# Performance work log

Hardware: AMD Instinct MI355X
Metric: run time of the kernel (lower is better)

Reference implementation:

```python
import jax, jax.numpy as jnp
import numpy as np

D = 2048
H = 16
DK = D // H
B = 2
S = 2048


def setup_inputs() -> dict:
    key = jax.random.key(0)
    ks = jax.random.split(key, 11)
    s = 1.0 / np.sqrt(D)
    inp = {
        "q": jax.random.normal(ks[0], (B, S, D), jnp.float32),
        "k": jax.random.normal(ks[1], (B, S, D), jnp.float32),
        "v": jax.random.normal(ks[2], (B, S, D), jnp.float32),
        "mask": 0,
        "Wq": jax.random.normal(ks[3], (D, D), jnp.float32) * s,
        "bq": jax.random.normal(ks[4], (D,), jnp.float32) * s,
        "Wk": jax.random.normal(ks[5], (D, D), jnp.float32) * s,
        "bk": jax.random.normal(ks[6], (D,), jnp.float32) * s,
        "Wv": jax.random.normal(ks[7], (D, D), jnp.float32) * s,
        "bv": jax.random.normal(ks[8], (D,), jnp.float32) * s,
        "Wo": jax.random.normal(ks[9], (D, D), jnp.float32) * s,
        "bo": jax.random.normal(ks[10], (D,), jnp.float32) * s,
    }
    return inp


def reference(q, k, v, mask, Wq, bq, Wk, bk, Wv, bv, Wo, bo):
    # Linear projections (torch Linear: x @ W.T + b)
    query = q @ Wq.T + bq  # [B,S,D]
    key_ = k @ Wk.T + bk
    value = v @ Wv.T + bv
    # split heads -> [B,S,H,DK]
    query = query.reshape(B, S, H, DK)
    key_ = key_.reshape(B, S, H, DK)
    value = value.reshape(B, S, H, DK)
    # scores [B,H,Sq,Sk]
    scores = jnp.einsum('nqhd,nkhd->nhqk', query, key_)
    if mask:
        # faithful to source: fill where triu(ones, diag=1) == 0 (lower tri incl diag)
        tri = jnp.triu(jnp.ones((S, S), jnp.float32), k=1)
        scores = jnp.where(tri == 0, jnp.float32(-1e20), scores)
    attn = jax.nn.softmax(scores / np.sqrt(DK), axis=3)
    # dropout=0.0 -> identity
    out = jnp.einsum('nhql,nlhd->nqhd', attn, value).reshape(B, S, D)
    return out @ Wo.T + bo
```

## Files before the change

kernel.cpp:

```cpp
#include <hip/hip_runtime.h>
#include <math.h>

typedef unsigned short u16;
typedef u16 u16x8 __attribute__((ext_vector_type(8)));
typedef u16 u16x4 __attribute__((ext_vector_type(4)));
typedef short s16x8 __attribute__((ext_vector_type(8)));
typedef short s16x4 __attribute__((ext_vector_type(4)));
typedef float f32x4 __attribute__((ext_vector_type(4)));

static constexpr int B_ = 2;
static constexpr int S_ = 2048;
static constexpr int D_ = 2048;
static constexpr int H_ = 16;
static constexpr int DK = 128;
static constexpr long long BSD = (long long)B_ * S_ * D_;
static constexpr long long DD  = (long long)D_ * D_;

#if __has_builtin(__builtin_amdgcn_mfma_f32_16x16x32_bf16)
#define HAVE_MFMA32 1
#else
#define HAVE_MFMA32 0
#endif
#if __has_builtin(__builtin_amdgcn_mfma_f32_16x16x16bf16_1k)
#define HAVE_MFMA16 1
#else
#define HAVE_MFMA16 0
#endif

__device__ __forceinline__ u16 f2bf(float f) {
    union { float f; unsigned u; } cv; cv.f = f;
    unsigned u = cv.u;
    return (u16)((u + 0x7fffu + ((u >> 16) & 1u)) >> 16);
}

__device__ __forceinline__ unsigned pack2bf(float a, float b) {
    union { float f; unsigned u; } x, y; x.f = a; y.f = b;
    return ((y.u + 0x8000u) & 0xffff0000u) | ((x.u + 0x8000u) >> 16);
}

__device__ __forceinline__ f32x4 mfma32(f32x4 c, u16x8 a, u16x8 b) {
#if HAVE_MFMA32
    return __builtin_amdgcn_mfma_f32_16x16x32_bf16((s16x8)a, (s16x8)b, c, 0, 0, 0);
#else
    asm volatile("v_mfma_f32_16x16x32_bf16 %0, %1, %2, %0" : "+v"(c) : "v"(a), "v"(b));
    return c;
#endif
}
__device__ __forceinline__ f32x4 mfma16(f32x4 c, u16x4 a, u16x4 b) {
#if HAVE_MFMA16
    return __builtin_amdgcn_mfma_f32_16x16x16bf16_1k((s16x4)a, (s16x4)b, c, 0, 0, 0);
#else
    asm volatile("v_mfma_f32_16x16x16_bf16 %0, %1, %2, %0" : "+v"(c) : "v"(a), "v"(b));
    return c;
#endif
}
__device__ __forceinline__ void fenceB() {
#if !HAVE_MFMA32 || !HAVE_MFMA16
    asm volatile("s_nop 7\ns_nop 7" :::);
#endif
}

__device__ __forceinline__ void glds16(const u16* g, u16* l) {
    __builtin_amdgcn_global_load_lds(
        (const __attribute__((address_space(1))) unsigned int*)g,
        (__attribute__((address_space(3))) unsigned int*)l, 16, 0, 0);
}

__device__ __forceinline__ float fexp2(float x) {
#if __has_builtin(__builtin_amdgcn_exp2f)
    return __builtin_amdgcn_exp2f(x);
#else
    return exp2f(x);
#endif
}

__device__ __forceinline__ void cfence() { asm volatile("" ::: "memory"); }
__device__ __forceinline__ void barrier8() {
    cfence();
    __builtin_amdgcn_s_barrier();
    cfence();
}
#define LGKM0() do { asm volatile("s_waitcnt lgkmcnt(0)" ::: "memory"); \
                     __builtin_amdgcn_sched_barrier(0); } while (0)
#define VMC(N)  asm volatile("s_waitcnt vmcnt(" #N ")" ::: "memory")

struct CastArgs {
    const float* src[7];
    u16* dst[7];
    int start[8];
};
__global__ __launch_bounds__(256) void cast_all(CastArgs a) {
    int g = blockIdx.x * 256 + threadIdx.x;
    if (g >= a.start[7]) return;
    int seg = 0;
#pragma unroll
    for (int i = 1; i < 7; ++i) seg += (g >= a.start[i]) ? 1 : 0;
    int idx = g - a.start[seg];
    float4 f = ((const float4*)a.src[seg])[idx];
    ushort4 o;
    o.x = f2bf(f.x); o.y = f2bf(f.y); o.z = f2bf(f.z); o.w = f2bf(f.w);
    ((ushort4*)a.dst[seg])[idx] = o;
}

#define GEMM_K64_LOOP(Aptr, Bptr)                                                   \
    for (int k0 = 0; k0 < D_; k0 += 64) {                                           \
        __syncthreads();                                                            \
        _Pragma("unroll")                                                           \
        for (int s = 0; s < 4; ++s) {                                               \
            int slot = s * 256 + t;                                                 \
            int row = slot >> 3;                                                    \
            int c = (t & 7) ^ (row & 7);                                            \
            glds16(Aptr + (m0 + row) * D_ + k0 + c * 8, &As[slot * 8]);             \
        }                                                                           \
        _Pragma("unroll")                                                           \
        for (int s = 0; s < 4; ++s) {                                               \
            int slot = s * 256 + t;                                                 \
            int row = slot >> 3;                                                    \
            int c = (t & 7) ^ (row & 7);                                            \
            glds16(Bptr + (n0 + row) * D_ + k0 + c * 8, &Bs[slot * 8]);             \
        }                                                                           \
        __syncthreads();                                                            \
        u16x8 af[4][2], bf[4][2];                                                   \
        _Pragma("unroll")                                                           \
        for (int i = 0; i < 4; ++i) {                                               \
            int row = wm + i * 16 + l16;                                            \
            _Pragma("unroll")                                                       \
            for (int kk = 0; kk < 2; ++kk)                                          \
                af[i][kk] = *(const u16x8*)(&As[row * 64 +                          \
                                (((kk * 4 + quad) ^ (row & 7)) * 8)]);              \
        }                                                                           \
        _Pragma("unroll")                                                           \
        for (int j = 0; j < 4; ++j) {                                               \
            int row = wn + j * 16 + l16;                                            \
            _Pragma("unroll")                                                       \
            for (int kk = 0; kk < 2; ++kk)                                          \
                bf[j][kk] = *(const u16x8*)(&Bs[row * 64 +                          \
                                (((kk * 4 + quad) ^ (row & 7)) * 8)]);              \
        }                                                                           \
        _Pragma("unroll")                                                           \
        for (int kk = 0; kk < 2; ++kk)                                              \
            _Pragma("unroll")                                                       \
            for (int i = 0; i < 4; ++i)                                             \
                _Pragma("unroll")                                                   \
                for (int j = 0; j < 4; ++j)                                         \
                    acc[i][j] = mfma32(acc[i][j], af[i][kk], bf[j][kk]);            \
    }

struct QkvArgs {
    const u16* X[3];
    const u16* W[3];
    const float* bias[3];
    u16* outQ;
    u16* outK;
    u16* outVt;
    float scaleQ;
};

#define STAGE_U(LDSP, GBASE)                                                        \
    _Pragma("unroll")                                                               \
    for (int jj = 0; jj < 2; ++jj) {                                                \
        int slot = jj * 512 + t;                                                    \
        int row = slot >> 3, c = slot & 7;                                          \
        glds16((GBASE) + (long long)row * D_ + ((c ^ (row & 7)) * 8),               \
               (LDSP) + slot * 8);                                                  \
    }

#define RD_K(kk, AsT, BsT)                                                          \
    _Pragma("unroll")                                                               \
    for (int i2 = 0; i2 < 4; ++i2) {                                                \
        int row = wm64 + i2 * 16 + l16;                                             \
        af2[i2] = *(const u16x8*)(&(AsT)[row * 64 +                                 \
                        ((((kk) * 4 + quad) ^ (row & 7)) * 8)]);                    \
    }                                                                               \
    _Pragma("unroll")                                                               \
    for (int j2 = 0; j2 < 4; ++j2) {                                                \
        int row = wn64 + j2 * 16 + l16;                                             \
        bf2[j2] = *(const u16x8*)(&(BsT)[row * 64 +                                 \
                        ((((kk) * 4 + quad) ^ (row & 7)) * 8)]);                    \
    }

#define MMK()                                                                       \
    __builtin_amdgcn_s_setprio(1);                                                  \
    _Pragma("unroll")                                                               \
    for (int i2 = 0; i2 < 4; ++i2)                                                  \
        _Pragma("unroll")                                                           \
        for (int j2 = 0; j2 < 4; ++j2)                                              \
            acc[i2][j2] = mfma32(acc[i2][j2], af2[i2], bf2[j2]);                    \
    __builtin_amdgcn_s_setprio(0);

__global__ __launch_bounds__(512, 2) void qkv_tri(QkvArgs a) {
    __shared__ u16 SM8[73728];
    u16* const Abase = SM8;
    u16* const Bbase = SM8 + 24576;

    const int l = blockIdx.x;
    const int f = (l & 7) * 96 + (l >> 3);
    const int zsel = f >> 8;
    const int r = f & 255;
    const int bx = r >> 5;
    const int by = r & 31;

    const u16* __restrict__ Ag = a.X[zsel];
    const u16* __restrict__ Bg = a.W[zsel];

    const int t = threadIdx.x;
    const int lane = t & 63;
    const int quad = lane >> 4, l16 = lane & 15;
    const int wave = t >> 6;
    const int wm64 = (wave >> 2) * 64;
    const int wn64 = (wave & 3) * 64;
    const long long m0 = (long long)by * 128;
    const long long n0 = (long long)bx * 256;

    f32x4 acc[4][4];
#pragma unroll
    for (int i = 0; i < 4; ++i)
#pragma unroll
        for (int j = 0; j < 4; ++j)
            acc[i][j] = f32x4{0.f, 0.f, 0.f, 0.f};

    u16x8 af2[4], bf2[4];

    STAGE_U(Abase,                Ag + m0 * D_)
    STAGE_U(Bbase,                Bg + n0 * D_)
    STAGE_U(Bbase + 8192,         Bg + (n0 + 128) * D_)
    STAGE_U(Abase + 8192,         Ag + m0 * D_ + 64)
    STAGE_U(Bbase + 16384,        Bg + n0 * D_ + 64)
    STAGE_U(Bbase + 16384 + 8192, Bg + (n0 + 128) * D_ + 64)
    VMC(6);
    barrier8();

    int eb = 0, ob = 1;
#pragma unroll 1
    for (int it = 0; it < 16; ++it) {
        const bool more = (it < 15);
        const long long kE2 = (long long)(2 * it + 2) * 64;
        const long long kO2 = kE2 + 64;
        const int en = (eb + 2 > 2) ? eb - 1 : eb + 2;

        u16* const AsE = Abase + eb * 8192;
        u16* const BsE = Bbase + eb * 16384;
        u16* const AsO = Abase + ob * 8192;
        u16* const BsO = Bbase + ob * 16384;
        u16* const AsnE = Abase + en * 8192;
        u16* const BsnE = Bbase + en * 16384;
        u16* const AsnO = AsE;
        u16* const BsnO = BsE;

        RD_K(0, AsE, BsE)
        if (more) {
            STAGE_U(AsnE, Ag + m0 * D_ + kE2)
            STAGE_U(BsnE, Bg + n0 * D_ + kE2)
        }
        barrier8(); LGKM0(); MMK() barrier8();

        RD_K(1, AsE, BsE)
        if (more) { STAGE_U(BsnE + 8192, Bg + (n0 + 128) * D_ + kE2) }
        barrier8(); LGKM0(); MMK()
        if (more) { VMC(6); } else { VMC(0); }
        barrier8();

        RD_K(0, AsO, BsO)
        if (more) {
            STAGE_U(AsnO, Ag + m0 * D_ + kO2)
            STAGE_U(BsnO, Bg + n0 * D_ + kO2)
        }
        barrier8(); LGKM0(); MMK() barrier8();

        RD_K(1, AsO, BsO)
        if (more) { STAGE_U(BsnO + 8192, Bg + (n0 + 128) * D_ + kO2) }
        barrier8(); LGKM0(); MMK()
        if (more) { VMC(6); }
        barrier8();

        eb = en;
        ob = (ob + 2 > 2) ? ob - 1 : ob + 2;
    }
    fenceB();

    float bs[4];
#pragma unroll
    for (int j = 0; j < 4; ++j)
        bs[j] = a.bias[zsel][(int)n0 + wn64 + j * 16 + l16];

    if (zsel < 2) {
        const float scale = (zsel == 0) ? a.scaleQ : 1.0f;
        u16* C = (zsel == 0) ? a.outQ : a.outK;
#pragma unroll
        for (int i = 0; i < 4; ++i)
#pragma unroll
            for (int j = 0; j < 4; ++j)
#pragma unroll
                for (int rr = 0; rr < 4; ++rr) {
                    int row = wm64 + i * 16 + quad * 4 + rr;
                    int col = wn64 + j * 16 + l16;
                    SM8[row * 256 + col] = f2bf((acc[i][j][rr] + bs[j]) * scale);
                }
        barrier8();
#pragma unroll
        for (int s = 0; s < 8; ++s) {
            int idx = s * 512 + t;
            int row = idx >> 5, c = idx & 31;
            *(u16x8*)(C + (m0 + row) * (long long)D_ + n0 + c * 8) =
                *(const u16x8*)(&SM8[row * 256 + c * 8]);
        }
    } else {
        const int h0 = (int)(n0 >> 7);
        const int bb = (int)(m0 >> 11);
        const int tok0 = (int)(m0 & 2047);
#pragma unroll
        for (int i = 0; i < 4; ++i)
#pragma unroll
            for (int j = 0; j < 4; ++j)
#pragma unroll
                for (int rr = 0; rr < 4; ++rr) {
                    int row = wm64 + i * 16 + quad * 4 + rr;
                    int d = wn64 + j * 16 + l16;
                    SM8[d * 136 + row] = f2bf(acc[i][j][rr] + bs[j]);
                }
        barrier8();
#pragma unroll
        for (int hh = 0; hh < 2; ++hh) {
            u16* vt = a.outVt + (long long)(bb * 16 + h0 + hh) * DK * S_;
#pragma unroll
            for (int s = 0; s < 4; ++s) {
                int idx = s * 512 + t;
                int d = idx >> 4, tc = idx & 15;
                *(u16x8*)(vt + (long long)d * S_ + tok0 + tc * 8) =
                    *(const u16x8*)(&SM8[(hh * 128 + d) * 136 + tc * 8]);
            }
        }
    }
}

__global__ __launch_bounds__(256) void gemm_out(const u16* __restrict__ Ain,
                                                const u16* __restrict__ Bin,
                                                float* __restrict__ C,
                                                const float* __restrict__ bias) {
    __shared__ u16 SM[16384];
    u16* As = SM;
    u16* Bs = SM + 8192;

    const int t = threadIdx.x;
    const int wave = t >> 6, lane = t & 63;
    const int quad = lane >> 4, l16 = lane & 15;
    const int wm = (wave >> 1) * 64;
    const int wn = (wave & 1) * 64;
    const long long m0 = (long long)blockIdx.y * 128;
    const long long n0 = (long long)blockIdx.x * 128;

    f32x4 acc[4][4];
#pragma unroll
    for (int i = 0; i < 4; ++i)
#pragma unroll
        for (int j = 0; j < 4; ++j)
            acc[i][j] = f32x4{0.f, 0.f, 0.f, 0.f};

    GEMM_K64_LOOP(Ain, Bin)

    fenceB();

    float bs[4];
#pragma unroll
    for (int j = 0; j < 4; ++j)
        bs[j] = bias[(int)n0 + wn + j * 16 + l16];

    float* Cf = (float*)SM;
#pragma unroll
    for (int p = 0; p < 2; ++p) {
        __syncthreads();
#pragma unroll
        for (int jj = 0; jj < 2; ++jj) {
            int j = p * 2 + jj;
#pragma unroll
            for (int i = 0; i < 4; ++i)
#pragma unroll
                for (int r = 0; r < 4; ++r) {
                    int row = wm + i * 16 + quad * 4 + r;
                    int lc = (wave & 1) * 32 + jj * 16 + l16;
                    Cf[row * 64 + lc] = acc[i][j][r] + bs[j];
                }
        }
        __syncthreads();
#pragma unroll
        for (int i = 0; i < 8; ++i) {
            int idx = i * 256 + t;
            int row = idx >> 4, c4 = idx & 15;
            f32x4 val = *(const f32x4*)(&Cf[row * 64 + c4 * 4]);
            long long n = n0 + (c4 >> 3) * 64 + p * 32 + (c4 & 7) * 4;
            *(f32x4*)(C + (m0 + row) * (long long)D_ + n) = val;
        }
    }
}

__global__ __launch_bounds__(256, 2) void flash_attn(const u16* __restrict__ Qb,
                                                     const u16* __restrict__ Kb,
                                                     const u16* __restrict__ Vt,
                                                     u16* __restrict__ Ob) {
    __shared__ u16 Ks[2][64 * 128];
    __shared__ u16 Vs[2][128 * 64];

    const int z  = blockIdx.x;
    const int qt = blockIdx.y;
    const int b  = z >> 4, h = z & 15;
    const int t = threadIdx.x, wave = t >> 6, lane = t & 63;
    const int quad = lane >> 4, l16 = lane & 15;

    const u16* kbase = Kb + (long long)(b * S_) * D_ + h * DK;
    const u16* vbase = Vt + (long long)z * DK * S_;

    u16x8 qf[2][4];
    {
        const u16* qbase = Qb + ((long long)(b * S_ + qt * 128 + wave * 32 + l16)) * D_
                              + h * DK + quad * 8;
#pragma unroll
        for (int jq = 0; jq < 2; ++jq)
#pragma unroll
            for (int kk = 0; kk < 4; ++kk)
                qf[jq][kk] = *(const u16x8*)(qbase + (long long)jq * 16 * D_ + kk * 32);
    }

    f32x4 acc_o[2][8];
#pragma unroll
    for (int jq = 0; jq < 2; ++jq)
#pragma unroll
        for (int jd = 0; jd < 8; ++jd)
            acc_o[jq][jd] = f32x4{0.f, 0.f, 0.f, 0.f};
    float l_[2] = {0.f, 0.f};

    u16x8 vreg[4];

    {
#pragma unroll
        for (int i = 0; i < 4; ++i) {
            int slot = i * 256 + t;
            int row = slot >> 3, c16 = slot & 7;
            vreg[i] = *(const u16x8*)(vbase + (long long)row * S_ + c16 * 8);
        }
#pragma unroll
        for (int i = 0; i < 4; ++i) {
            int slot = i * 256 + t;
            int row = slot >> 4;
            int cs = (slot & 15) ^ (row & 7);
            glds16(kbase + (long long)row * D_ + cs * 8, &Ks[0][slot * 8]);
        }
#pragma unroll
        for (int i = 0; i < 4; ++i) {
            int slot = i * 256 + t;
            int row = slot >> 3, c16 = slot & 7;
            int rm = row & 15;
            u16x4 lo = __builtin_shufflevector(vreg[i], vreg[i], 0, 1, 2, 3);
            u16x4 hi = __builtin_shufflevector(vreg[i], vreg[i], 4, 5, 6, 7);
            *(u16x4*)(&Vs[0][row * 64 + (((2 * c16) ^ rm) * 4)]) = lo;
            *(u16x4*)(&Vs[0][row * 64 + (((2 * c16 + 1) ^ rm) * 4)]) = hi;
        }
    }

    for (int kt = 0; kt < S_ / 64; ++kt) {
        __syncthreads();
        const int p = kt & 1;
        const u16* ks = Ks[p];
        const u16* vs = Vs[p];
        const bool pre = (kt + 1) < (S_ / 64);
        if (pre) {
            const u16* vsrc = vbase + (kt + 1) * 64;
#pragma unroll
            for (int i = 0; i < 4; ++i) {
                int slot = i * 256 + t;
                int row = slot >> 3, c16 = slot & 7;
                vreg[i] = *(const u16x8*)(vsrc + (long long)row * S_ + c16 * 8);
            }
            const u16* ksrc = kbase + (long long)(kt + 1) * 64 * D_;
#pragma unroll
            for (int i = 0; i < 4; ++i) {
                int slot = i * 256 + t;
                int row = slot >> 4;
                int cs = (slot & 15) ^ (row & 7);
                glds16(ksrc + (long long)row * D_ + cs * 8, &Ks[p ^ 1][slot * 8]);
            }
        }

        f32x4 st[4][2];
#pragma unroll
        for (int ik = 0; ik < 4; ++ik)
#pragma unroll
            for (int jq = 0; jq < 2; ++jq)
                st[ik][jq] = f32x4{0.f, 0.f, 0.f, 0.f};
#pragma unroll
        for (int kk = 0; kk < 4; ++kk) {
            u16x8 kf[4];
#pragma unroll
            for (int ik = 0; ik < 4; ++ik) {
                int krow = ik * 16 + l16;
                kf[ik] = *(const u16x8*)(&ks[krow * 128 + (((kk * 4 + quad) ^ (l16 & 7)) * 8)]);
            }
#pragma unroll
            for (int ik = 0; ik < 4; ++ik) {
                st[ik][0] = mfma32(st[ik][0], kf[ik], qf[0][kk]);
                st[ik][1] = mfma32(st[ik][1], kf[ik], qf[1][kk]);
            }
        }
        fenceB();

        if (pre) {
#pragma unroll
            for (int i = 0; i < 4; ++i) {
                int slot = i * 256 + t;
                int row = slot >> 3, c16 = slot & 7;
                int rm = row & 15;
                u16x4 lo = __builtin_shufflevector(vreg[i], vreg[i], 0, 1, 2, 3);
                u16x4 hi = __builtin_shufflevector(vreg[i], vreg[i], 4, 5, 6, 7);
                *(u16x4*)(&Vs[p ^ 1][row * 64 + (((2 * c16) ^ rm) * 4)]) = lo;
                *(u16x4*)(&Vs[p ^ 1][row * 64 + (((2 * c16 + 1) ^ rm) * 4)]) = hi;
            }
        }

        u16x4 pf[4][2];
#pragma unroll
        for (int ik = 0; ik < 4; ++ik)
#pragma unroll
            for (int jq = 0; jq < 2; ++jq) {
                float p0 = fexp2(st[ik][jq][0]);
                float p1 = fexp2(st[ik][jq][1]);
                float p2 = fexp2(st[ik][jq][2]);
                float p3 = fexp2(st[ik][jq][3]);
                l_[jq] += (p0 + p1) + (p2 + p3);
                union { u16x4 v; unsigned u[2]; } pk;
                pk.u[0] = pack2bf(p0, p1);
                pk.u[1] = pack2bf(p2, p3);
                pf[ik][jq] = pk.v;
            }

#pragma unroll
        for (int ik = 0; ik < 4; ++ik) {
            const int kc = ik * 4 + quad;
            u16x4 vf[8];
#pragma unroll
            for (int jd = 0; jd < 8; ++jd) {
                int vrow = jd * 16 + l16;
                vf[jd] = *(const u16x4*)(&vs[vrow * 64 + ((kc ^ l16) * 4)]);
            }
#pragma unroll
            for (int jd = 0; jd < 8; ++jd) {
                acc_o[0][jd] = mfma16(acc_o[0][jd], pf[ik][0], vf[jd]);
                acc_o[1][jd] = mfma16(acc_o[1][jd], pf[ik][1], vf[jd]);
            }
        }
        fenceB();
    }

    float lr[2][4];
#pragma unroll
    for (int jq = 0; jq < 2; ++jq) {
        float s = l_[jq];
        s += __shfl_xor(s, 16, 64);
        s += __shfl_xor(s, 32, 64);
        float inv = 1.f / s;
#pragma unroll
        for (int r = 0; r < 4; ++r)
            lr[jq][r] = __shfl(inv, quad * 20 + r, 64);
    }
    u16* OS = (u16*)Ks;
    __syncthreads();
#pragma unroll
    for (int jq = 0; jq < 2; ++jq)
#pragma unroll
        for (int r = 0; r < 4; ++r) {
            int qloc = wave * 32 + jq * 16 + quad * 4 + r;
#pragma unroll
            for (int jd = 0; jd < 8; ++jd)
                OS[qloc * 128 + jd * 16 + l16] = f2bf(acc_o[jq][jd][r] * lr[jq][r]);
        }
    __syncthreads();
    u16* obase = Ob + ((long long)(b * S_ + qt * 128)) * D_ + h * DK;
#pragma unroll
    for (int i = 0; i < 8; ++i) {
        int idx = i * 256 + t;
        int row = idx >> 4, cc = idx & 15;
        *(u16x8*)(obase + (long long)row * D_ + cc * 8) = *(const u16x8*)(&OS[row * 128 + cc * 8]);
    }
}

extern "C" void kernel_launch(void* const* d_in, const int* in_sizes, int n_in,
                              void* d_out, int out_size, void* d_ws, size_t ws_size,
                              hipStream_t stream) {
    const float* q  = (const float*)d_in[0];
    const float* k  = (const float*)d_in[1];
    const float* v  = (const float*)d_in[2];
    const float* Wq = (const float*)d_in[4];
    const float* bq = (const float*)d_in[5];
    const float* Wk = (const float*)d_in[6];
    const float* bk = (const float*)d_in[7];
    const float* Wv = (const float*)d_in[8];
    const float* bv = (const float*)d_in[9];
    const float* Wo = (const float*)d_in[10];
    const float* bo = (const float*)d_in[11];
    float* out = (float*)d_out;

    u16* ws = (u16*)d_ws;
    u16* xq  = ws; ws += BSD;
    u16* xk  = ws; ws += BSD;
    u16* xv  = ws; ws += BSD;
    u16* wqb = ws; ws += DD;
    u16* wkb = ws; ws += DD;
    u16* wvb = ws; ws += DD;
    u16* wob = ws; ws += DD;
    u16* Qb  = ws; ws += BSD;
    u16* Kb  = ws; ws += BSD;
    u16* Vt  = ws; ws += BSD;
    u16* Ob  = ws; ws += BSD;

    const float q_scale = (float)(0.08838834764831845 * 1.4426950408889634);

    {
        CastArgs a;
        const float* srcs[7] = {q, k, v, Wq, Wk, Wv, Wo};
        u16* dsts[7] = {xq, xk, xv, wqb, wkb, wvb, wob};
        int n4s[7] = {(int)(BSD / 4), (int)(BSD / 4), (int)(BSD / 4),
                      (int)(DD / 4), (int)(DD / 4), (int)(DD / 4), (int)(DD / 4)};
        int acc = 0;
        for (int i = 0; i < 7; ++i) { a.src[i] = srcs[i]; a.dst[i] = dsts[i]; a.start[i] = acc; acc += n4s[i]; }
        a.start[7] = acc;
        cast_all<<<(acc + 255) / 256, 256, 0, stream>>>(a);
    }

    {
        QkvArgs a;
        a.X[0] = xq;  a.X[1] = xk;  a.X[2] = xv;
        a.W[0] = wqb; a.W[1] = wkb; a.W[2] = wvb;
        a.bias[0] = bq; a.bias[1] = bk; a.bias[2] = bv;
        a.outQ = Qb; a.outK = Kb; a.outVt = Vt;
        a.scaleQ = q_scale;
        qkv_tri<<<dim3(768, 1, 1), 512, 0, stream>>>(a);
    }

    flash_attn<<<dim3(B_ * H_, S_ / 128), 256, 0, stream>>>(Qb, Kb, Vt, Ob);

    gemm_out<<<dim3(D_ / 128, (B_ * S_) / 128), 256, 0, stream>>>(Ob, wob, out, bo);
}
```

Baseline: 434.3 us.

## Share a leaner triple-buffered GEMM mainloop between QKV and output projections

Replaces the QKV GEMM's unrolled two-phase loop, which had many barriers, with a shared macro body. The body uses one barrier per K-step, precomputed swizzled LDS offsets, incremented global pointers, and a three-stage async-copy pipeline. The output projection moves from a simple single-buffered 128x128 GEMM with 256 threads to the same 128x256, 512-thread pipelined body with a grouped block-index remap for L2 locality. It trades larger LDS use and lower occupancy for fewer synchronizations and better load/compute overlap.

```diff
diff --git a/kernel.cpp b/kernel.cpp
--- a/kernel.cpp
+++ b/kernel.cpp
@@ -80,9 +80,8 @@
     __builtin_amdgcn_s_barrier();
     cfence();
 }
-#define LGKM0() do { asm volatile("s_waitcnt lgkmcnt(0)" ::: "memory"); \
-                     __builtin_amdgcn_sched_barrier(0); } while (0)
 #define VMC(N)  asm volatile("s_waitcnt vmcnt(" #N ")" ::: "memory")
+#define LGKMB() do { asm volatile("s_waitcnt lgkmcnt(0)" ::: "memory"); barrier8(); } while (0)
 
 struct CastArgs {
     const float* src[7];
@@ -102,49 +101,107 @@
     ((ushort4*)a.dst[seg])[idx] = o;
 }
 
-#define GEMM_K64_LOOP(Aptr, Bptr)                                                   \
-    for (int k0 = 0; k0 < D_; k0 += 64) {                                           \
-        __syncthreads();                                                            \
+
+#define ABYTE(s) ((s) * 16384)
+#define BBYTE(s) (49152 + (s) * 32768)
+
+#define STAGE_TILE(SA, SB)                                                          \
+    glds16(pA0, SMu + ((SA) >> 1) + d0);                                            \
+    glds16(pA1, SMu + ((SA) >> 1) + d1);                                            \
+    glds16(pB00, SMu + ((SB) >> 1) + d0);                                           \
+    glds16(pB01, SMu + ((SB) >> 1) + d1);                                           \
+    glds16(pB10, SMu + ((SB) >> 1) + 8192 + d0);                                    \
+    glds16(pB11, SMu + ((SB) >> 1) + 8192 + d1);                                    \
+    pA0 += 64; pA1 += 64; pB00 += 64; pB01 += 64; pB10 += 64; pB11 += 64;
+
+#define LD8(BOFF) (*(const u16x8*)(SMc + (BOFF)))
+
+#define RD_FRAGS(SA, SB)                                                            \
+    _Pragma("unroll")                                                               \
+    for (int i2 = 0; i2 < 4; ++i2) {                                                \
+        afA[i2] = LD8((SA) + offA[i2]);                                             \
+        afB[i2] = LD8((SA) + (offA[i2] ^ 64));                                      \
+    }                                                                               \
+    _Pragma("unroll")                                                               \
+    for (int j2 = 0; j2 < 4; ++j2) {                                                \
+        bfA[j2] = LD8((SB) + offB[j2]);                                             \
+        bfB[j2] = LD8((SB) + (offB[j2] ^ 64));                                      \
+    }
+
+#define MMALL()                                                                     \
+    __builtin_amdgcn_s_setprio(1);                                                  \
+    _Pragma("unroll")                                                               \
+    for (int i2 = 0; i2 < 4; ++i2)                                                  \
         _Pragma("unroll")                                                           \
-        for (int s = 0; s < 4; ++s) {                                               \
-            int slot = s * 256 + t;                                                 \
-            int row = slot >> 3;                                                    \
-            int c = (t & 7) ^ (row & 7);                                            \
-            glds16(Aptr + (m0 + row) * D_ + k0 + c * 8, &As[slot * 8]);             \
-        }                                                                           \
+        for (int j2 = 0; j2 < 4; ++j2)                                              \
+            acc[i2][j2] = mfma32(acc[i2][j2], afA[i2], bfA[j2]);                    \
+    _Pragma("unroll")                                                               \
+    for (int i2 = 0; i2 < 4; ++i2)                                                  \
         _Pragma("unroll")                                                           \
-        for (int s = 0; s < 4; ++s) {                                               \
-            int slot = s * 256 + t;                                                 \
-            int row = slot >> 3;                                                    \
-            int c = (t & 7) ^ (row & 7);                                            \
-            glds16(Bptr + (n0 + row) * D_ + k0 + c * 8, &Bs[slot * 8]);             \
-        }                                                                           \
-        __syncthreads();                                                            \
-        u16x8 af[4][2], bf[4][2];                                                   \
+        for (int j2 = 0; j2 < 4; ++j2)                                              \
+            acc[i2][j2] = mfma32(acc[i2][j2], afB[i2], bfB[j2]);                    \
+    __builtin_amdgcn_s_setprio(0);
+
+#define GEMM_LEAN_BODY(AGPTR, BGPTR)                                                \
+    u16* const SMu = SM8;                                                           \
+    const char* const SMc = (const char*)SM8;                                       \
+    const int t = threadIdx.x;                                                      \
+    const int lane = t & 63;                                                        \
+    const int quad = lane >> 4, l16 = lane & 15;                                    \
+    const int wave = t >> 6;                                                        \
+    const int wm64 = (wave >> 2) * 64;                                              \
+    const int wn64 = (wave & 3) * 64;                                               \
+    const long long m0 = (long long)by * 128;                                       \
+    const long long n0 = (long long)bx * 256;                                       \
+    const int tr = t >> 3, tc = t & 7;                                              \
+    const int swz = (tc ^ (tr & 7)) * 8;                                            \
+    const u16* pA0  = (AGPTR) + (m0 + tr) * D_ + swz;                               \
+    const u16* pA1  = (AGPTR) + (m0 + 64 + tr) * D_ + swz;                          \
+    const u16* pB00 = (BGPTR) + (n0 + tr) * D_ + swz;                               \
+    const u16* pB01 = (BGPTR) + (n0 + 64 + tr) * D_ + swz;                          \
+    const u16* pB10 = (BGPTR) + (n0 + 128 + tr) * D_ + swz;                         \
+    const u16* pB11 = (BGPTR) + (n0 + 192 + tr) * D_ + swz;                         \
+    const int d0 = t * 8, d1 = t * 8 + 4096;                                        \
+    int offA[4], offB[4];                                                           \
+    _Pragma("unroll")                                                               \
+    for (int i2 = 0; i2 < 4; ++i2) {                                                \
+        int rowA = wm64 + i2 * 16 + l16;                                            \
+        offA[i2] = rowA * 128 + ((quad ^ (rowA & 7)) << 4);                         \
+        int rowB = wn64 + i2 * 16 + l16;                                            \
+        offB[i2] = rowB * 128 + ((quad ^ (rowB & 7)) << 4);                         \
+    }                                                                               \
+    f32x4 acc[4][4];                                                                \
+    _Pragma("unroll")                                                               \
+    for (int i = 0; i < 4; ++i)                                                     \
         _Pragma("unroll")                                                           \
-        for (int i = 0; i < 4; ++i) {                                               \
-            int row = wm + i * 16 + l16;                                            \
-            _Pragma("unroll")                                                       \
-            for (int kk = 0; kk < 2; ++kk)                                          \
-                af[i][kk] = *(const u16x8*)(&As[row * 64 +                          \
-                                (((kk * 4 + quad) ^ (row & 7)) * 8)]);              \
-        }                                                                           \
-        _Pragma("unroll")                                                           \
-        for (int j = 0; j < 4; ++j) {                                               \
-            int row = wn + j * 16 + l16;                                            \
-            _Pragma("unroll")                                                       \
-            for (int kk = 0; kk < 2; ++kk)                                          \
-                bf[j][kk] = *(const u16x8*)(&Bs[row * 64 +                          \
-                                (((kk * 4 + quad) ^ (row & 7)) * 8)]);              \
-        }                                                                           \
-        _Pragma("unroll")                                                           \
-        for (int kk = 0; kk < 2; ++kk)                                              \
-            _Pragma("unroll")                                                       \
-            for (int i = 0; i < 4; ++i)                                             \
-                _Pragma("unroll")                                                   \
-                for (int j = 0; j < 4; ++j)                                         \
-                    acc[i][j] = mfma32(acc[i][j], af[i][kk], bf[j][kk]);            \
-    }
+        for (int j = 0; j < 4; ++j)                                                 \
+            acc[i][j] = f32x4{0.f, 0.f, 0.f, 0.f};                                  \
+    u16x8 afA[4], afB[4], bfA[4], bfB[4];                                           \
+                                            \
+    STAGE_TILE(ABYTE(0), BBYTE(0))                                                  \
+    STAGE_TILE(ABYTE(1), BBYTE(1))                                                  \
+    VMC(6);                                                                         \
+    barrier8();                                                                     \
+    _Pragma("unroll 3")                                                             \
+    for (int kt = 0; kt < 30; ++kt) {                                               \
+        const int s = kt % 3;                                                       \
+        const int s2 = (kt + 2) % 3;                                                \
+        RD_FRAGS(ABYTE(s), BBYTE(s))                                                \
+        STAGE_TILE(ABYTE(s2), BBYTE(s2))                                            \
+        MMALL()                                                                     \
+        VMC(6);                                                                     \
+        LGKMB();                                                                    \
+    }                                                                               \
+                             \
+    RD_FRAGS(ABYTE(0), BBYTE(0))                                                    \
+    MMALL()                                                                         \
+    VMC(0);                                                                         \
+    LGKMB();                                                                        \
+                                                              \
+    RD_FRAGS(ABYTE(1), BBYTE(1))                                                    \
+    MMALL()                                                                         \
+    LGKMB();                                                                        \
+    fenceB();
 
 struct QkvArgs {
     const u16* X[3];
@@ -156,127 +213,20 @@
     float scaleQ;
 };
 
-#define STAGE_U(LDSP, GBASE)                                                        \
-    _Pragma("unroll")                                                               \
-    for (int jj = 0; jj < 2; ++jj) {                                                \
-        int slot = jj * 512 + t;                                                    \
-        int row = slot >> 3, c = slot & 7;                                          \
-        glds16((GBASE) + (long long)row * D_ + ((c ^ (row & 7)) * 8),               \
-               (LDSP) + slot * 8);                                                  \
-    }
-
-#define RD_K(kk, AsT, BsT)                                                          \
-    _Pragma("unroll")                                                               \
-    for (int i2 = 0; i2 < 4; ++i2) {                                                \
-        int row = wm64 + i2 * 16 + l16;                                             \
-        af2[i2] = *(const u16x8*)(&(AsT)[row * 64 +                                 \
-                        ((((kk) * 4 + quad) ^ (row & 7)) * 8)]);                    \
-    }                                                                               \
-    _Pragma("unroll")                                                               \
-    for (int j2 = 0; j2 < 4; ++j2) {                                                \
-        int row = wn64 + j2 * 16 + l16;                                             \
-        bf2[j2] = *(const u16x8*)(&(BsT)[row * 64 +                                 \
-                        ((((kk) * 4 + quad) ^ (row & 7)) * 8)]);                    \
-    }
-
-#define MMK()                                                                       \
-    __builtin_amdgcn_s_setprio(1);                                                  \
-    _Pragma("unroll")                                                               \
-    for (int i2 = 0; i2 < 4; ++i2)                                                  \
-        _Pragma("unroll")                                                           \
-        for (int j2 = 0; j2 < 4; ++j2)                                              \
-            acc[i2][j2] = mfma32(acc[i2][j2], af2[i2], bf2[j2]);                    \
-    __builtin_amdgcn_s_setprio(0);
-
-__global__ __launch_bounds__(512, 2) void qkv_tri(QkvArgs a) {
+__global__ __launch_bounds__(512, 2) void qkv_lean(QkvArgs a) {
     __shared__ u16 SM8[73728];
-    u16* const Abase = SM8;
-    u16* const Bbase = SM8 + 24576;
 
     const int l = blockIdx.x;
-    const int f = (l & 7) * 96 + (l >> 3);
-    const int zsel = f >> 8;
-    const int r = f & 255;
-    const int bx = r >> 5;
-    const int by = r & 31;
+    const int zsel = l >> 8;
+    const int pi = l & 7;
+    const int cc_ = (l >> 3) & 31;
+    const int by = (pi & 3) * 8 + (cc_ & 7);
+    const int bx = ((pi >> 2) << 2) + (cc_ >> 3);
 
     const u16* __restrict__ Ag = a.X[zsel];
     const u16* __restrict__ Bg = a.W[zsel];
 
-    const int t = threadIdx.x;
-    const int lane = t & 63;
-    const int quad = lane >> 4, l16 = lane & 15;
-    const int wave = t >> 6;
-    const int wm64 = (wave >> 2) * 64;
-    const int wn64 = (wave & 3) * 64;
-    const long long m0 = (long long)by * 128;
-    const long long n0 = (long long)bx * 256;
-
-    f32x4 acc[4][4];
-#pragma unroll
-    for (int i = 0; i < 4; ++i)
-#pragma unroll
-        for (int j = 0; j < 4; ++j)
-            acc[i][j] = f32x4{0.f, 0.f, 0.f, 0.f};
-
-    u16x8 af2[4], bf2[4];
-
-    STAGE_U(Abase,                Ag + m0 * D_)
-    STAGE_U(Bbase,                Bg + n0 * D_)
-    STAGE_U(Bbase + 8192,         Bg + (n0 + 128) * D_)
-    STAGE_U(Abase + 8192,         Ag + m0 * D_ + 64)
-    STAGE_U(Bbase + 16384,        Bg + n0 * D_ + 64)
-    STAGE_U(Bbase + 16384 + 8192, Bg + (n0 + 128) * D_ + 64)
-    VMC(6);
-    barrier8();
-
-    int eb = 0, ob = 1;
-#pragma unroll 1
-    for (int it = 0; it < 16; ++it) {
-        const bool more = (it < 15);
-        const long long kE2 = (long long)(2 * it + 2) * 64;
-        const long long kO2 = kE2 + 64;
-        const int en = (eb + 2 > 2) ? eb - 1 : eb + 2;
-
-        u16* const AsE = Abase + eb * 8192;
-        u16* const BsE = Bbase + eb * 16384;
-        u16* const AsO = Abase + ob * 8192;
-        u16* const BsO = Bbase + ob * 16384;
-        u16* const AsnE = Abase + en * 8192;
-        u16* const BsnE = Bbase + en * 16384;
-        u16* const AsnO = AsE;
-        u16* const BsnO = BsE;
-
-        RD_K(0, AsE, BsE)
-        if (more) {
-            STAGE_U(AsnE, Ag + m0 * D_ + kE2)
-            STAGE_U(BsnE, Bg + n0 * D_ + kE2)
-        }
-        barrier8(); LGKM0(); MMK() barrier8();
-
-        RD_K(1, AsE, BsE)
-        if (more) { STAGE_U(BsnE + 8192, Bg + (n0 + 128) * D_ + kE2) }
-        barrier8(); LGKM0(); MMK()
-        if (more) { VMC(6); } else { VMC(0); }
-        barrier8();
-
-        RD_K(0, AsO, BsO)
-        if (more) {
-            STAGE_U(AsnO, Ag + m0 * D_ + kO2)
-            STAGE_U(BsnO, Bg + n0 * D_ + kO2)
-        }
-        barrier8(); LGKM0(); MMK() barrier8();
-
-        RD_K(1, AsO, BsO)
-        if (more) { STAGE_U(BsnO + 8192, Bg + (n0 + 128) * D_ + kO2) }
-        barrier8(); LGKM0(); MMK()
-        if (more) { VMC(6); }
-        barrier8();
-
-        eb = en;
-        ob = (ob + 2 > 2) ? ob - 1 : ob + 2;
-    }
-    fenceB();
+    GEMM_LEAN_BODY(Ag, Bg)
 
     float bs[4];
 #pragma unroll
@@ -325,70 +275,57 @@
 #pragma unroll
             for (int s = 0; s < 4; ++s) {
                 int idx = s * 512 + t;
-                int d = idx >> 4, tc = idx & 15;
-                *(u16x8*)(vt + (long long)d * S_ + tok0 + tc * 8) =
-                    *(const u16x8*)(&SM8[(hh * 128 + d) * 136 + tc * 8]);
-            }
-        }
-    }
-}
-
-__global__ __launch_bounds__(256) void gemm_out(const u16* __restrict__ Ain,
-                                                const u16* __restrict__ Bin,
-                                                float* __restrict__ C,
-                                                const float* __restrict__ bias) {
-    __shared__ u16 SM[16384];
-    u16* As = SM;
-    u16* Bs = SM + 8192;
-
-    const int t = threadIdx.x;
-    const int wave = t >> 6, lane = t & 63;
-    const int quad = lane >> 4, l16 = lane & 15;
-    const int wm = (wave >> 1) * 64;
-    const int wn = (wave & 1) * 64;
-    const long long m0 = (long long)blockIdx.y * 128;
-    const long long n0 = (long long)blockIdx.x * 128;
-
-    f32x4 acc[4][4];
-#pragma unroll
-    for (int i = 0; i < 4; ++i)
-#pragma unroll
-        for (int j = 0; j < 4; ++j)
-            acc[i][j] = f32x4{0.f, 0.f, 0.f, 0.f};
-
-    GEMM_K64_LOOP(Ain, Bin)
-
-    fenceB();
+                int d = idx >> 4, tcc = idx & 15;
+                *(u16x8*)(vt + (long long)d * S_ + tok0 + tcc * 8) =
+                    *(const u16x8*)(&SM8[(hh * 128 + d) * 136 + tcc * 8]);
+            }
+        }
+    }
+}
+
+__global__ __launch_bounds__(512, 2) void gemm_out_lean(const u16* __restrict__ Ain,
+                                                        const u16* __restrict__ Bin,
+                                                        float* __restrict__ C,
+                                                        const float* __restrict__ bias) {
+    __shared__ u16 SM8[73728];
+
+    const int l = blockIdx.x;
+    const int pi = l & 7;
+    const int cc_ = (l >> 3) & 31;
+    const int by = (pi & 3) * 8 + (cc_ & 7);
+    const int bx = ((pi >> 2) << 2) + (cc_ >> 3);
+
+    GEMM_LEAN_BODY(Ain, Bin)
 
     float bs[4];
 #pragma unroll
     for (int j = 0; j < 4; ++j)
-        bs[j] = bias[(int)n0 + wn + j * 16 + l16];
-
-    float* Cf = (float*)SM;
+        bs[j] = bias[(int)n0 + wn64 + j * 16 + l16];
+
+    float* Cf = (float*)SM8;
 #pragma unroll
     for (int p = 0; p < 2; ++p) {
-        __syncthreads();
-#pragma unroll
-        for (int jj = 0; jj < 2; ++jj) {
-            int j = p * 2 + jj;
+        barrier8();
+        if (((wave & 3) >> 1) == p) {
+            int wnl = (wave & 1) * 64;
 #pragma unroll
             for (int i = 0; i < 4; ++i)
 #pragma unroll
-                for (int r = 0; r < 4; ++r) {
-                    int row = wm + i * 16 + quad * 4 + r;
-                    int lc = (wave & 1) * 32 + jj * 16 + l16;
-                    Cf[row * 64 + lc] = acc[i][j][r] + bs[j];
-                }
-        }
-        __syncthreads();
-#pragma unroll
-        for (int i = 0; i < 8; ++i) {
-            int idx = i * 256 + t;
-            int row = idx >> 4, c4 = idx & 15;
-            f32x4 val = *(const f32x4*)(&Cf[row * 64 + c4 * 4]);
-            long long n = n0 + (c4 >> 3) * 64 + p * 32 + (c4 & 7) * 4;
-            *(f32x4*)(C + (m0 + row) * (long long)D_ + n) = val;
+                for (int j = 0; j < 4; ++j)
+#pragma unroll
+                    for (int rr = 0; rr < 4; ++rr) {
+                        int row = wm64 + i * 16 + quad * 4 + rr;
+                        int lc = wnl + j * 16 + l16;
+                        Cf[row * 128 + lc] = acc[i][j][rr] + bs[j];
+                    }
+        }
+        barrier8();
+#pragma unroll
+        for (int s = 0; s < 8; ++s) {
+            int idx = s * 512 + t;
+            int row = idx >> 5, c4 = idx & 31;
+            f32x4 val = *(const f32x4*)(&Cf[row * 128 + c4 * 4]);
+            *(f32x4*)(C + (m0 + row) * (long long)D_ + n0 + p * 128 + c4 * 4) = val;
         }
     }
 }
@@ -631,10 +568,10 @@
         a.bias[0] = bq; a.bias[1] = bk; a.bias[2] = bv;
         a.outQ = Qb; a.outK = Kb; a.outVt = Vt;
         a.scaleQ = q_scale;
-        qkv_tri<<<dim3(768, 1, 1), 512, 0, stream>>>(a);
+        qkv_lean<<<dim3(768, 1, 1), 512, 0, stream>>>(a);
     }
 
     flash_attn<<<dim3(B_ * H_, S_ / 128), 256, 0, stream>>>(Qb, Kb, Vt, Ob);
 
-    gemm_out<<<dim3(D_ / 128, (B_ * S_) / 128), 256, 0, stream>>>(Ob, wob, out, bo);
-}
+    gemm_out_lean<<<dim3(256, 1, 1), 512, 0, stream>>>(Ob, wob, out, bo);
+}
```

After: 428.2 us. No clear change (-1.4%).
